# Kernel tuning notes

Measured on AMD Instinct MI355X. Metric: run time of the kernel, lower is better.

Reference implementation:

```python
import jax, jax.numpy as jnp
import numpy as np

DIM = 1024
HEADS = 8
KV_HEADS = 1
GROUPS = HEADS // KV_HEADS
D_QK = 128
D_V = 192
DIM_PAIRWISE = 128
SCALE = 64 ** -0.5  # module uses dim_head=64 for scale, not dim_head_qk
SOFTCLAMP = 5.0
RMS_EPS = 1.1920929e-07  # torch nn.RMSNorm default eps = float32 machine eps
BN_EPS = 1e-05


def setup_inputs() -> dict:
    key = jax.random.key(0)
    ks = jax.random.split(key, 12)
    b, n, i = 1, 2048, 512
    qkv_out = HEADS * D_QK + D_QK + D_V  # 1344
    inv = lambda fan_in: 1.0 / np.sqrt(fan_in)
    return {
        "x": jax.random.normal(ks[0], (b, n, DIM), jnp.float32),
        "pairwise": jax.random.normal(ks[1], (b, i, i, DIM_PAIRWISE), jnp.float32),
        "rotary_emb": jax.random.normal(ks[2], (n, D_QK), jnp.float32),
        "W_qkv": jax.random.normal(ks[3], (DIM, qkv_out), jnp.float32) * inv(DIM),
        "q_norm_w": jnp.ones((D_QK,), jnp.float32),
        "k_norm_w": jnp.ones((D_QK,), jnp.float32),
        "v_norm_w": jnp.ones((D_V,), jnp.float32),
        "bn_gamma": jax.random.normal(ks[4], (DIM_PAIRWISE,), jnp.float32) * 0.02,
        "bn_beta": jax.random.normal(ks[5], (DIM_PAIRWISE,), jnp.float32) * 0.02,
        "bn_running_var": jnp.ones((DIM_PAIRWISE,), jnp.float32),
        "W_bias": jax.random.normal(ks[6], (DIM_PAIRWISE, HEADS), jnp.float32) * inv(DIM_PAIRWISE),
        "W_out": jax.random.normal(ks[7], (HEADS * D_V, DIM), jnp.float32) * inv(HEADS * D_V),
    }


def _rmsnorm(t, w):
    var = jnp.mean(jnp.square(t), axis=-1, keepdims=True)
    return t * jax.lax.rsqrt(var + RMS_EPS) * w


def _rotate_half(t):
    t1, t2 = jnp.split(t, 2, axis=-1)
    return jnp.concatenate((-t2, t1), axis=-1)


def _apply_rope(pos, t):
    return t * jnp.cos(pos) + _rotate_half(t) * jnp.sin(pos)


def reference(x, pairwise, rotary_emb, W_qkv, q_norm_w, k_norm_w, v_norm_w,
              bn_gamma, bn_beta, bn_running_var, W_bias, W_out):
    b, n, _ = x.shape
    qkv = x @ W_qkv
    q, k, v = jnp.split(qkv, [HEADS * D_QK, HEADS * D_QK + D_QK], axis=-1)

    # q: b n (g h d) -> b g h n d ; k,v: b n (h d) -> b h n d
    q = q.reshape(b, n, GROUPS, KV_HEADS, D_QK).transpose(0, 2, 3, 1, 4)
    k = k.reshape(b, n, KV_HEADS, D_QK).transpose(0, 2, 1, 3)
    v = v.reshape(b, n, KV_HEADS, D_V).transpose(0, 2, 1, 3)

    q = _rmsnorm(q, q_norm_w) * SCALE
    k = _rmsnorm(k, k_norm_w)
    v = _rmsnorm(v, v_norm_w)

    q = _apply_rope(rotary_emb, q)
    k = _apply_rope(rotary_emb, k)

    sim = jnp.einsum('bghid,bhjd->bghij', q, k)

    # pairwise attn bias: BatchRMSNorm (eval) -> GELU -> Linear -> b g h i j
    std = jnp.sqrt(jnp.clip(bn_running_var, BN_EPS, None))
    pw = pairwise / std * (DIM_PAIRWISE ** 0.5)
    pw = pw * (bn_gamma + 1.0) + bn_beta
    pw = jax.nn.gelu(pw, approximate=False)
    attn_bias = pw @ W_bias  # [b, i, j, heads]
    bi = attn_bias.shape[1]
    attn_bias = attn_bias.reshape(b, bi, bi, GROUPS, KV_HEADS).transpose(0, 3, 4, 1, 2)

    r = n // bi  # expand_factor
    attn_bias = jnp.repeat(jnp.repeat(attn_bias, r, axis=-2), r, axis=-1)

    sim = jnp.tanh((sim + attn_bias) / SOFTCLAMP) * SOFTCLAMP
    attn = jax.nn.softmax(sim, axis=-1)

    out = jnp.einsum('bghij,bhjd->bghid', attn, v)
    out = out.transpose(0, 3, 1, 2, 4).reshape(b, n, GROUPS * KV_HEADS * D_V)
    return out @ W_out
```

## Files before the change

kernel.cpp:

```cpp
#include <hip/hip_runtime.h>
#include <math.h>

typedef unsigned short u16;
typedef __attribute__((ext_vector_type(4))) float f32x4;
typedef __attribute__((ext_vector_type(8))) short s16x8;
typedef __attribute__((ext_vector_type(8))) _Float16 f16x8;

__device__ __forceinline__ u16 f2bf(float f){
  unsigned u = __builtin_bit_cast(unsigned, f);
  u += 0x7fffu + ((u >> 16) & 1u);
  return (u16)(u >> 16);
}
__device__ __forceinline__ float bf2f(u16 h){
  unsigned u = ((unsigned)h) << 16;
  return __builtin_bit_cast(float, u);
}
__device__ __forceinline__ u16 f2h(float f){
  return __builtin_bit_cast(u16, (_Float16)f);
}
__device__ __forceinline__ float h2f(u16 h){
  return (float)__builtin_bit_cast(_Float16, h);
}
__device__ __forceinline__ f32x4 mfma16h(f16x8 a, f16x8 b, f32x4 c){
  return __builtin_amdgcn_mfma_f32_16x16x32_f16(a, b, c, 0, 0, 0);
}
__device__ __forceinline__ void gload16(const void* src, const u16* ldsbase){
  __builtin_amdgcn_global_load_lds(
      (const __attribute__((address_space(1))) void*)src,
      (__attribute__((address_space(3))) void*)ldsbase, 16, 0, 0);
}

__global__ __launch_bounds__(256) void k_pre(const float* __restrict__ x,
    const float* __restrict__ Wq, const float* __restrict__ Wo,
    u16* __restrict__ Afq, u16* __restrict__ Bq1, u16* __restrict__ Bq2){
  __shared__ float tile[64][65];
  int b = blockIdx.x, t = threadIdx.x;
  if (b < 1024){
    int id = b*256 + t;
    int row = id>>7, k0 = (id&127)*8;
    const float4* xp = (const float4*)(x + (size_t)row*1024 + k0);
    float4 v0 = xp[0], v1 = xp[1];
    float vv[8] = {v0.x,v0.y,v0.z,v0.w, v1.x,v1.y,v1.z,v1.w};
    u16 hh[8];
    #pragma unroll
    for (int e=0; e<8; ++e) hh[e] = f2h(vv[e]);
    int mt = row>>7, ms = (row>>4)&7, m16 = row&15;
    int kt = k0>>6, ks2 = (k0>>5)&1, lg = (k0>>3)&3;
    int lane = lg*16 + m16;
    size_t base = (size_t)(mt*16 + kt)*8192;
    *(uint4*)&Afq[base + (size_t)(ks2*8 + ms)*512 + lane*8] = *(uint4*)hh;
    return;
  }
  const float* in; u16* Bfq; int N, nKt, nt, kt;
  if (b < 1360){
    int bb = b - 1024; nt = bb % 21; kt = bb / 21;
    in = Wq; Bfq = Bq1; N = 1344; nKt = 16;
  } else {
    int bb = b - 1360; nt = bb % 16; kt = bb / 16;
    in = Wo; Bfq = Bq2; N = 1024; nKt = 24;
  }
  #pragma unroll
  for (int i=0; i<16; ++i){
    int idx = i*256 + t;
    int r = idx>>6, c = idx&63;
    tile[r][c] = in[(size_t)(kt*64 + r)*N + nt*64 + c];
  }
  __syncthreads();
  size_t base = (size_t)(nt*nKt + kt)*4096;
  #pragma unroll
  for (int j=0; j<2; ++j){
    int idx = j*256 + t;
    int np = idx>>3, ko = idx&7;
    u16 hh[8];
    #pragma unroll
    for (int e=0; e<8; ++e) hh[e] = f2h(tile[ko*8+e][np]);
    int ks2 = ko>>2, lg = ko&3, ns = np>>4, n16 = np&15;
    int lane = lg*16 + n16;
    *(uint4*)&Bfq[base + (size_t)(ks2*4 + ns)*512 + lane*8] = *(uint4*)hh;
  }
}

__global__ __launch_bounds__(256,3) void k_g1b(const u16* __restrict__ Afq,
    const u16* __restrict__ Bq1, u16* __restrict__ qkvh,
    const float* __restrict__ pw, const float* __restrict__ rv,
    const float* __restrict__ gamma, const float* __restrict__ beta,
    const float* __restrict__ Wb, u16* __restrict__ biash){
  __shared__ u16 lds[24576];
  int b = blockIdx.x, t = threadIdx.x;
  int w = t>>6, lane = t&63, lg = lane>>4, lr = lane&15;
  if (b < 336){
    int id2 = (b & 7)*42 + (b >> 3);
    int by = id2 / 21, bx = id2 - by*21;
    int iw = w&1, jw = w>>1;
    int n0 = bx*64, m0 = by*128;
    const char* srcA = (const char*)(Afq + (size_t)by*16*8192);
    const char* srcB = (const char*)(Bq1 + (size_t)bx*16*4096);
    int wb = w*1024 + lane*16;
    auto stage = [&](int kt, int cur){
      const char* ta = srcA + (size_t)kt*16384;
      const char* tb = srcB + (size_t)kt*8192;
      int ab = cur*12288;
      #pragma unroll
      for (int i=0; i<4; ++i)
        gload16(ta + i*4096 + wb, &lds[ab + ((i*4096 + w*1024)>>1)]);
      #pragma unroll
      for (int i=0; i<2; ++i)
        gload16(tb + i*4096 + wb, &lds[ab + 8192 + ((i*4096 + w*1024)>>1)]);
    };
    f32x4 acc[4][2] = {};
    stage(0, 0);
    __syncthreads();
    int cur = 0;
    for (int kt=0; kt<16; ++kt){
      if (kt+1 < 16) stage(kt+1, cur^1);
      int ab = cur*12288;
      #pragma unroll
      for (int ks2=0; ks2<2; ++ks2){
        f16x8 ah[4], bh[2];
        #pragma unroll
        for (int m=0; m<4; ++m)
          ah[m] = *(const f16x8*)&lds[ab + (size_t)(ks2*8 + iw*4 + m)*512 + lane*8];
        #pragma unroll
        for (int n=0; n<2; ++n)
          bh[n] = *(const f16x8*)&lds[ab + 8192 + (size_t)(ks2*4 + jw*2 + n)*512 + lane*8];
        #pragma unroll
        for (int m=0; m<4; ++m)
          #pragma unroll
          for (int n=0; n<2; ++n)
            acc[m][n] = mfma16h(ah[m], bh[n], acc[m][n]);
      }
      __syncthreads();
      cur ^= 1;
    }
    #pragma unroll
    for (int m=0; m<4; ++m)
      #pragma unroll
      for (int n=0; n<2; ++n)
        #pragma unroll
        for (int r=0; r<4; ++r){
          int row = m0 + iw*64 + m*16 + lg*4 + r;
          int col = n0 + jw*32 + n*16 + lr;
          qkvh[(size_t)row*1344 + col] = f2h(acc[m][n][r]);
        }
    return;
  }
  int bb = b - 336;
  float* As = (float*)lds;
  float* Bs = As + 128;
  if (t < 128){
    As[t] = 11.313708498984761f * rsqrtf(fmaxf(rv[t], 1e-5f)) * (gamma[t] + 1.0f);
    Bs[t] = beta[t];
  }
  __syncthreads();
  f16x8 wbf[4];
  #pragma unroll
  for (int ks=0; ks<4; ++ks){
    f16x8 vh;
    #pragma unroll
    for (int e=0; e<8; ++e){
      float v = (lr < 8) ? Wb[(ks*32 + lg*8 + e)*8 + lr] : 0.0f;
      vh[e] = (_Float16)v;
    }
    wbf[ks] = vh;
  }
  #pragma unroll
  for (int it=0; it<2; ++it){
    int p0 = bb*128 + it*64 + w*16;
    const float* rowp = pw + (size_t)(p0 + lr)*128;
    f32x4 acc = {0.f,0.f,0.f,0.f};
    #pragma unroll
    for (int ks=0; ks<4; ++ks){
      int c = ks*32 + lg*8;
      float4 x0 = *(const float4*)(rowp + c);
      float4 x1 = *(const float4*)(rowp + c + 4);
      float4 a0 = *(const float4*)&As[c], a1 = *(const float4*)&As[c+4];
      float4 b0 = *(const float4*)&Bs[c], b1 = *(const float4*)&Bs[c+4];
      float xv[8] = {x0.x*a0.x+b0.x, x0.y*a0.y+b0.y, x0.z*a0.z+b0.z, x0.w*a0.w+b0.w,
                     x1.x*a1.x+b1.x, x1.y*a1.y+b1.y, x1.z*a1.z+b1.z, x1.w*a1.w+b1.w};
      f16x8 gh;
      #pragma unroll
      for (int e=0; e<8; ++e){
        float v = xv[e];
        float z = v * 0.7071067811865476f;
        float s = fabsf(z);
        float tt = 1.0f / (1.0f + 0.3275911f*s);
        float poly = ((((1.061405429f*tt - 1.453152027f)*tt + 1.421413741f)*tt - 0.284496736f)*tt + 0.254829592f)*tt;
        float E = __expf(-s*s);
        float Q = 0.5f*v*poly*E;
        float ge = (v >= 0.0f) ? (v - Q) : Q;
        gh[e] = (_Float16)ge;
      }
      acc = mfma16h(gh, wbf[ks], acc);
    }
    if (lr < 8)
      #pragma unroll
      for (int r=0; r<4; ++r)
        biash[(size_t)(p0 + lg*4 + r)*8 + lr] = f2h(acc[r]);
  }
}

__global__ __launch_bounds__(256) void k_norm(const u16* __restrict__ qkvh,
   const float* __restrict__ rot, const float* __restrict__ qw, const float* __restrict__ kw,
   const float* __restrict__ vw, u16* __restrict__ Qf, u16* __restrict__ KVF){
  int t = threadIdx.x;
  int w = t>>6, l = t&63;
  int task = blockIdx.x*4 + w;
  int n = task/10, g = task - (task/10)*10;
  const u16* row = qkvh + (size_t)n*1344;
  size_t tbase = (size_t)(n>>5)*10240;
  if (g < 9){
    float e0 = h2f(row[g*128 + l]);
    float e1 = h2f(row[g*128 + 64 + l]);
    float s = e0*e0 + e1*e1;
    #pragma unroll
    for (int m=1; m<64; m<<=1) s += __shfl_xor(s, m, 64);
    float rr = rsqrtf(s*(1.0f/128.0f) + 1.1920929e-07f);
    const float* ww = (g < 8) ? qw : kw;
    float sc = (g < 8) ? 0.125f : 1.0f;
    float qn0 = e0*rr*ww[l]*sc;
    float qn1 = e1*rr*ww[64+l]*sc;
    float p0 = rot[(size_t)n*128 + l], p1 = rot[(size_t)n*128 + 64 + l];
    float c0, s0, c1, s1;
    __sincosf(p0, &s0, &c0);
    __sincosf(p1, &s1, &c1);
    float o0 = qn0*c0 - qn1*s0;
    float o1 = qn1*c1 + qn0*s1;
    if (g < 8){
      Qf[((size_t)g*2048 + n)*128 + l]      = f2h(o0);
      Qf[((size_t)g*2048 + n)*128 + 64 + l] = f2h(o1);
    } else {
      int d0 = l, d1 = 64 + l;
      size_t ka0 = tbase + (size_t)((d0>>5)*2 + ((n>>4)&1))*512
                 + (size_t)(((d0>>3)&3)*16 + (n&15))*8 + (d0&7);
      size_t ka1 = tbase + (size_t)((d1>>5)*2 + ((n>>4)&1))*512
                 + (size_t)(((d1>>3)&3)*16 + (n&15))*8 + (d1&7);
      KVF[ka0] = f2h(o0);
      KVF[ka1] = f2h(o1);
    }
  } else {
    float v0 = h2f(row[1152 + l]);
    float v1 = h2f(row[1152 + 64 + l]);
    float v2 = h2f(row[1152 + 128 + l]);
    float s = v0*v0 + v1*v1 + v2*v2;
    #pragma unroll
    for (int m=1; m<64; m<<=1) s += __shfl_xor(s, m, 64);
    float rr = rsqrtf(s*(1.0f/192.0f) + 1.1920929e-07f);
    int lgv = (n>>3)&3, ev = n&7;
    size_t vbase = tbase + 4096;
    float vals[3] = {v0, v1, v2};
    #pragma unroll
    for (int j=0; j<3; ++j){
      int d = j*64 + l;
      KVF[vbase + (size_t)(d>>4)*512 + (size_t)(lgv*16 + (d&15))*8 + ev]
          = f2h(vals[j]*rr*vw[d]);
    }
  }
}

__global__ __launch_bounds__(256,3) void k_gemm2(const u16* __restrict__ Afq,
    const u16* __restrict__ Bfq, void* __restrict__ Cv, int N, int nKt, int halfOut, int NX){
  __shared__ u16 lds[24576];
  int id = blockIdx.x;
  int per = gridDim.x >> 3;
  int id2 = (id & 7)*per + (id >> 3);
  int by = id2 / NX;
  int bx = id2 - by*NX;
  int t = threadIdx.x;
  int w = t>>6, lane = t&63, lg = lane>>4, lr = lane&15;
  int iw = w&1, jw = w>>1;
  int n0 = bx*64, m0 = by*128;
  const char* srcA = (const char*)(Afq + (size_t)by*nKt*8192);
  const char* srcB = (const char*)(Bfq + (size_t)bx*nKt*4096);
  int wb = w*1024 + lane*16;
  auto stage = [&](int kt, int cur){
    const char* ta = srcA + (size_t)kt*16384;
    const char* tb = srcB + (size_t)kt*8192;
    int ab = cur*12288;
    #pragma unroll
    for (int i=0; i<4; ++i)
      gload16(ta + i*4096 + wb, &lds[ab + ((i*4096 + w*1024)>>1)]);
    #pragma unroll
    for (int i=0; i<2; ++i)
      gload16(tb + i*4096 + wb, &lds[ab + 8192 + ((i*4096 + w*1024)>>1)]);
  };
  f32x4 acc[4][2] = {};
  stage(0, 0);
  __syncthreads();
  int cur = 0;
  for (int kt=0; kt<nKt; ++kt){
    if (kt+1 < nKt) stage(kt+1, cur^1);
    int ab = cur*12288;
    #pragma unroll
    for (int ks2=0; ks2<2; ++ks2){
      f16x8 ah[4], bh[2];
      #pragma unroll
      for (int m=0; m<4; ++m)
        ah[m] = *(const f16x8*)&lds[ab + (size_t)(ks2*8 + iw*4 + m)*512 + lane*8];
      #pragma unroll
      for (int n=0; n<2; ++n)
        bh[n] = *(const f16x8*)&lds[ab + 8192 + (size_t)(ks2*4 + jw*2 + n)*512 + lane*8];
      #pragma unroll
      for (int m=0; m<4; ++m)
        #pragma unroll
        for (int n=0; n<2; ++n)
          acc[m][n] = mfma16h(ah[m], bh[n], acc[m][n]);
    }
    __syncthreads();
    cur ^= 1;
  }
  #pragma unroll
  for (int m=0; m<4; ++m)
    #pragma unroll
    for (int n=0; n<2; ++n)
      #pragma unroll
      for (int r=0; r<4; ++r){
        int row = m0 + iw*64 + m*16 + lg*4 + r;
        int col = n0 + jw*32 + n*16 + lr;
        if (halfOut) ((u16*)Cv)[(size_t)row*N + col] = f2h(acc[m][n][r]);
        else         ((float*)Cv)[(size_t)row*N + col] = acc[m][n][r];
      }
}

__global__ __launch_bounds__(256,2) void k_attn6(const u16* __restrict__ Qf,
  const u16* __restrict__ KVF, const u16* __restrict__ biash,
  u16* __restrict__ OP, float* __restrict__ SP){
  __shared__ u16 lds[24576];
  int t = threadIdx.x;
  int w = t>>6, lane = t&63, lg = lane>>4, lr = lane&15;
  int q0 = blockIdx.x*32;
  int h  = blockIdx.y*4 + w;
  int zi = blockIdx.z;
  f16x8 qf[2][4];
  #pragma unroll
  for (int qi=0; qi<2; ++qi){
    const u16* qb = Qf + ((size_t)h*2048 + q0 + qi*16 + lr)*128 + lg*8;
    #pragma unroll
    for (int ks=0; ks<4; ++ks) qf[qi][ks] = *(const f16x8*)(qb + ks*32);
  }
  const char* kvb = (const char*)KVF + (size_t)zi*16*20480;
  int wb = w*1024 + lane*16;
  auto stage = [&](int jt, int cur){
    const char* src = kvb + (size_t)jt*20480;
    gload16(src + wb,         &lds[cur*4096 + (w*1024>>1)]);
    gload16(src + 4096 + wb,  &lds[cur*4096 + 2048 + (w*1024>>1)]);
    gload16(src + 8192 + wb,  &lds[8192 + cur*6144 + (w*1024>>1)]);
    gload16(src + 12288 + wb, &lds[8192 + cur*6144 + 2048 + (w*1024>>1)]);
    gload16(src + 16384 + wb, &lds[8192 + cur*6144 + 4096 + (w*1024>>1)]);
  };
  float bCur[2][2], bNxt[2][2];
  auto loadBias = [&](int jt, float bb[2][2]){
    int jq = (zi*512 + jt*32)>>2;
    #pragma unroll
    for (int qi=0; qi<2; ++qi)
      #pragma unroll
      for (int kj=0; kj<2; ++kj)
        bb[qi][kj] = 0.4f*h2f(biash[((size_t)((q0>>2) + qi*4 + lg)*512 + jq + kj*4 + (lr>>2))*8 + h]);
  };
  stage(0, 0);
  loadBias(0, bCur);
  __syncthreads();
  f32x4 accO[2][12] = {};
  f32x4 accR[2] = {};
  f16x8 vone;
  #pragma unroll
  for (int e=0; e<8; ++e) vone[e] = (_Float16)1.0f;
  int psb = 20480 + w*1024;
  int po0 = lane*8;       po0 ^= ((po0>>6)&7)<<3;
  int po1 = 512 + lane*8; po1 ^= ((po1>>6)&7)<<3;
  int cur = 0;
  for (int jt=0; jt<16; ++jt){
    if (jt < 15){ stage(jt+1, cur^1); loadBias(jt+1, bNxt); }
    f32x4 accS[2][2] = {};
    #pragma unroll
    for (int ks=0; ks<4; ++ks){
      #pragma unroll
      for (int kj=0; kj<2; ++kj){
        f16x8 kb = *(const f16x8*)&lds[cur*4096 + (ks*2+kj)*512 + lane*8];
        accS[0][kj] = mfma16h(qf[0][ks], kb, accS[0][kj]);
        accS[1][kj] = mfma16h(qf[1][ks], kb, accS[1][kj]);
      }
    }
    #pragma unroll
    for (int qi=0; qi<2; ++qi)
      #pragma unroll
      for (int kj=0; kj<2; ++kj){
        float bv = bCur[qi][kj];
        #pragma unroll
        for (int r=0; r<4; ++r){
          float te = __expf(0.4f*accS[qi][kj][r] + bv);
          float ri; asm("v_rcp_f32 %0, %1" : "=v"(ri) : "v"(te + 1.0f));
          float p = __expf(-10.0f*ri);
          int o = qi*512 + ((kj*2 + (lr>>3))*16 + lg*4 + r)*8 + (lr&7);
          o ^= ((o>>6)&7)<<3;
          lds[psb + o] = f2h(p);
        }
      }
    f16x8 pa0 = *(const f16x8*)&lds[psb + po0];
    f16x8 pa1 = *(const f16x8*)&lds[psb + po1];
    #pragma unroll
    for (int df=0; df<12; ++df){
      f16x8 vb = *(const f16x8*)&lds[8192 + cur*6144 + df*512 + lane*8];
      accO[0][df] = mfma16h(pa0, vb, accO[0][df]);
      accO[1][df] = mfma16h(pa1, vb, accO[1][df]);
    }
    accR[0] = mfma16h(pa0, vone, accR[0]);
    accR[1] = mfma16h(pa1, vone, accR[1]);
    __syncthreads();
    cur ^= 1;
    #pragma unroll
    for (int qi=0; qi<2; ++qi){ bCur[qi][0] = bNxt[qi][0]; bCur[qi][1] = bNxt[qi][1]; }
  }
  #pragma unroll
  for (int qi=0; qi<2; ++qi){
    #pragma unroll
    for (int df=0; df<12; ++df)
      #pragma unroll
      for (int r=0; r<4; ++r){
        int q = q0 + qi*16 + lg*4 + r;
        OP[(((size_t)zi*8 + h)*2048 + q)*192 + df*16 + lr] = f2h(accO[qi][df][r]);
      }
    if (lr == 0)
      #pragma unroll
      for (int r=0; r<4; ++r)
        SP[((size_t)zi*8 + h)*2048 + q0 + qi*16 + lg*4 + r] = accR[qi][r];
  }
}

__global__ __launch_bounds__(256) void k_comb2(const u16* __restrict__ OP,
    const float* __restrict__ SP, u16* __restrict__ Ao2){
  int id = blockIdx.x*256 + threadIdx.x;
  int hq = id / 24;
  int oct = id - hq*24;
  int d0 = oct*8;
  float inv = 1.0f / (SP[hq] + SP[16384+hq] + SP[32768+hq] + SP[49152+hq]);
  float o[8] = {0,0,0,0,0,0,0,0};
  #pragma unroll
  for (int z=0; z<4; ++z){
    uint4 v = *(const uint4*)&OP[((size_t)z*16384 + hq)*192 + d0];
    const u16* pv = (const u16*)&v;
    #pragma unroll
    for (int e=0; e<8; ++e) o[e] += h2f(pv[e]);
  }
  int h = hq >> 11, q = hq & 2047;
  int col = h*192 + d0;
  int kt = col>>6, ks2 = (col>>5)&1, lg = (col>>3)&3;
  int mt = q>>7, ms = (q>>4)&7, m16 = q&15;
  int lane = lg*16 + m16;
  u16 hh[8];
  #pragma unroll
  for (int e=0; e<8; ++e) hh[e] = f2h(o[e]*inv);
  size_t base = (size_t)(mt*24 + kt)*8192;
  *(uint4*)&Ao2[base + (size_t)(ks2*8 + ms)*512 + lane*8] = *(uint4*)hh;
}

extern "C" void kernel_launch(void* const* d_in, const int* in_sizes, int n_in,
                              void* d_out, int out_size, void* d_ws, size_t ws_size,
                              hipStream_t stream){
  (void)in_sizes; (void)n_in; (void)out_size; (void)ws_size;
  const float* x   = (const float*)d_in[0];
  const float* pwi = (const float*)d_in[1];
  const float* rot = (const float*)d_in[2];
  const float* Wq  = (const float*)d_in[3];
  const float* qw  = (const float*)d_in[4];
  const float* kw  = (const float*)d_in[5];
  const float* vw  = (const float*)d_in[6];
  const float* gm  = (const float*)d_in[7];
  const float* bt  = (const float*)d_in[8];
  const float* rvv = (const float*)d_in[9];
  const float* Wb  = (const float*)d_in[10];
  const float* Wo  = (const float*)d_in[11];
  float* out = (float*)d_out;
  char* ws = (char*)d_ws;
  size_t off = 0;
  auto alloc = [&](size_t bytes)->char*{
    char* p = ws + off; off = (off + bytes + 255) & ~(size_t)255; return p;
  };
  u16*   Axq = (u16*)alloc(16ull*16*8192*2);
  u16*   Bq1 = (u16*)alloc(21ull*16*4096*2);
  u16*   Bq2 = (u16*)alloc(16ull*24*4096*2);
  u16*   Ao2 = (u16*)alloc(16ull*24*8192*2);
  u16*   qkvh = (u16*)alloc(2048ull*1344*2);
  u16*   Qfb = (u16*)alloc(8ull*2048*128*2);
  u16*   KVF = (u16*)alloc(64ull*10240*2);
  u16*   biash = (u16*)alloc(8ull*512*512*2);
  u16*   OP  = (u16*)alloc(4ull*8*2048*192*2);
  float* SP  = (float*)alloc(4ull*8*2048*4);

  k_pre<<<1744, 256, 0, stream>>>(x, Wq, Wo, Axq, Bq1, Bq2);
  k_g1b<<<2384, 256, 0, stream>>>(Axq, Bq1, qkvh, pwi, rvv, gm, bt, Wb, biash);
  k_norm<<<5120, 256, 0, stream>>>(qkvh, rot, qw, kw, vw, Qfb, KVF);
  k_attn6<<<dim3(64, 2, 4), 256, 0, stream>>>(Qfb, KVF, biash, OP, SP);
  k_comb2<<<1536, 256, 0, stream>>>(OP, SP, Ao2);
  k_gemm2<<<256, 256, 0, stream>>>(Ao2, Bq2, out, 1024, 24, 0, 16);
}
```

Measured before the change: 131.6 us.

## Single-buffer LDS in fused GEMM/bias kernel, stage Wb in LDS, tanh-form GELU

The QKV GEMM path drops double-buffered LDS staging for a single buffer with a sync before and after each load, halving LDS use and raising launch bounds to allow more resident blocks. The pairwise-bias path stages the fp16 Wb fragments in LDS instead of registers. It also replaces the erf polynomial GELU with a sigmoid-form tanh approximation using a hardware reciprocal. The aim is more occupancy and less ALU work, at the cost of losing load/compute overlap in the GEMM and a small numerical deviation in GELU.

After: 110.1 us. -16.3%, faster.

```diff
diff --git a/kernel.cpp b/kernel.cpp
--- a/kernel.cpp
+++ b/kernel.cpp
@@ -80,12 +80,12 @@
   }
 }
 
-__global__ __launch_bounds__(256,3) void k_g1b(const u16* __restrict__ Afq,
+__global__ __launch_bounds__(256,6) void k_g1b2(const u16* __restrict__ Afq,
     const u16* __restrict__ Bq1, u16* __restrict__ qkvh,
     const float* __restrict__ pw, const float* __restrict__ rv,
     const float* __restrict__ gamma, const float* __restrict__ beta,
     const float* __restrict__ Wb, u16* __restrict__ biash){
-  __shared__ u16 lds[24576];
+  __shared__ u16 lds[12288];
   int b = blockIdx.x, t = threadIdx.x;
   int w = t>>6, lane = t&63, lg = lane>>4, lr = lane&15;
   if (b < 336){
@@ -96,41 +96,33 @@
     const char* srcA = (const char*)(Afq + (size_t)by*16*8192);
     const char* srcB = (const char*)(Bq1 + (size_t)bx*16*4096);
     int wb = w*1024 + lane*16;
-    auto stage = [&](int kt, int cur){
+    f32x4 acc[4][2] = {};
+    for (int kt=0; kt<16; ++kt){
+      __syncthreads();
       const char* ta = srcA + (size_t)kt*16384;
       const char* tb = srcB + (size_t)kt*8192;
-      int ab = cur*12288;
       #pragma unroll
       for (int i=0; i<4; ++i)
-        gload16(ta + i*4096 + wb, &lds[ab + ((i*4096 + w*1024)>>1)]);
+        gload16(ta + i*4096 + wb, &lds[(i*4096 + w*1024)>>1]);
       #pragma unroll
       for (int i=0; i<2; ++i)
-        gload16(tb + i*4096 + wb, &lds[ab + 8192 + ((i*4096 + w*1024)>>1)]);
-    };
-    f32x4 acc[4][2] = {};
-    stage(0, 0);
-    __syncthreads();
-    int cur = 0;
-    for (int kt=0; kt<16; ++kt){
-      if (kt+1 < 16) stage(kt+1, cur^1);
-      int ab = cur*12288;
+        gload16(tb + i*4096 + wb, &lds[8192 + ((i*4096 + w*1024)>>1)]);
+      __syncthreads();
       #pragma unroll
       for (int ks2=0; ks2<2; ++ks2){
         f16x8 ah[4], bh[2];
         #pragma unroll
         for (int m=0; m<4; ++m)
-          ah[m] = *(const f16x8*)&lds[ab + (size_t)(ks2*8 + iw*4 + m)*512 + lane*8];
+          ah[m] = *(const f16x8*)&lds[(size_t)(ks2*8 + iw*4 + m)*512 + lane*8];
         #pragma unroll
         for (int n=0; n<2; ++n)
-          bh[n] = *(const f16x8*)&lds[ab + 8192 + (size_t)(ks2*4 + jw*2 + n)*512 + lane*8];
+          bh[n] = *(const f16x8*)&lds[8192 + (size_t)(ks2*4 + jw*2 + n)*512 + lane*8];
         #pragma unroll
         for (int m=0; m<4; ++m)
           #pragma unroll
           for (int n=0; n<2; ++n)
             acc[m][n] = mfma16h(ah[m], bh[n], acc[m][n]);
       }
-      __syncthreads();
-      cur ^= 1;
     }
     #pragma unroll
     for (int m=0; m<4; ++m)
@@ -147,22 +139,20 @@
   int bb = b - 336;
   float* As = (float*)lds;
   float* Bs = As + 128;
+  u16* WbS = (u16*)(Bs + 128);
   if (t < 128){
     As[t] = 11.313708498984761f * rsqrtf(fmaxf(rv[t], 1e-5f)) * (gamma[t] + 1.0f);
     Bs[t] = beta[t];
   }
+  {
+    int ks = t>>6, lane2 = t&63, lg2 = lane2>>4, lr2 = lane2&15;
+    #pragma unroll
+    for (int e=0; e<8; ++e){
+      float v = (lr2 < 8) ? Wb[(ks*32 + lg2*8 + e)*8 + lr2] : 0.0f;
+      WbS[ks*512 + lane2*8 + e] = f2h(v);
+    }
+  }
   __syncthreads();
-  f16x8 wbf[4];
-  #pragma unroll
-  for (int ks=0; ks<4; ++ks){
-    f16x8 vh;
-    #pragma unroll
-    for (int e=0; e<8; ++e){
-      float v = (lr < 8) ? Wb[(ks*32 + lg*8 + e)*8 + lr] : 0.0f;
-      vh[e] = (_Float16)v;
-    }
-    wbf[ks] = vh;
-  }
   #pragma unroll
   for (int it=0; it<2; ++it){
     int p0 = bb*128 + it*64 + w*16;
@@ -181,16 +171,15 @@
       #pragma unroll
       for (int e=0; e<8; ++e){
         float v = xv[e];
-        float z = v * 0.7071067811865476f;
-        float s = fabsf(z);
-        float tt = 1.0f / (1.0f + 0.3275911f*s);
-        float poly = ((((1.061405429f*tt - 1.453152027f)*tt + 1.421413741f)*tt - 0.284496736f)*tt + 0.254829592f)*tt;
-        float E = __expf(-s*s);
-        float Q = 0.5f*v*poly*E;
-        float ge = (v >= 0.0f) ? (v - Q) : Q;
+        float u2 = v*v;
+        float arg = v*(1.5957691216f + 0.0713548162f*u2);
+        float te = __expf(arg);
+        float ri; asm("v_rcp_f32 %0, %1" : "=v"(ri) : "v"(te + 1.0f));
+        float ge = v - v*ri;
         gh[e] = (_Float16)ge;
       }
-      acc = mfma16h(gh, wbf[ks], acc);
+      f16x8 bh = *(const f16x8*)&WbS[ks*512 + lane*8];
+      acc = mfma16h(gh, bh, acc);
     }
     if (lr < 8)
       #pragma unroll
@@ -487,7 +476,7 @@
   float* SP  = (float*)alloc(4ull*8*2048*4);
 
   k_pre<<<1744, 256, 0, stream>>>(x, Wq, Wo, Axq, Bq1, Bq2);
-  k_g1b<<<2384, 256, 0, stream>>>(Axq, Bq1, qkvh, pwi, rvv, gm, bt, Wb, biash);
+  k_g1b2<<<2384, 256, 0, stream>>>(Axq, Bq1, qkvh, pwi, rvv, gm, bt, Wb, biash);
   k_norm<<<5120, 256, 0, stream>>>(qkvh, rot, qw, kw, vw, Qfb, KVF);
   k_attn6<<<dim3(64, 2, 4), 256, 0, stream>>>(Qfb, KVF, biash, OP, SP);
   k_comb2<<<1536, 256, 0, stream>>>(OP, SP, Ao2);
```
